# Optimization experiments

Measured on AMD Instinct MI355X. Metric: run time of the kernel, lower is better.

Reference implementation:

```python
import jax, jax.numpy as jnp
import numpy as np

N_NODES = 100000
N_EDGES = 1000000
IN_DIM = 64
HID = 64
N_CLUSTER = 30
REG = 0.01


def glorot(key, shape):
    lim = np.sqrt(6.0 / (shape[0] + shape[1]))
    return jax.random.uniform(key, shape, jnp.float32, -lim, lim)


def setup_inputs() -> dict:
    key = jax.random.key(0)
    k1, k2, k3, k4, k5 = jax.random.split(key, 5)
    x = jax.random.normal(k1, (N_NODES, IN_DIM), jnp.float32)
    edge_index = jax.random.randint(k2, (2, N_EDGES), 0, N_NODES, jnp.int64)
    edge_attr = jax.random.uniform(k3, (N_EDGES,), jnp.float32)
    W1 = glorot(k4, (IN_DIM, HID))
    b1 = jnp.zeros((HID,), jnp.float32)
    W2 = glorot(k5, (HID, N_CLUSTER))
    b2 = jnp.zeros((N_CLUSTER,), jnp.float32)
    return {"x": x, "edge_index": edge_index, "edge_attr": edge_attr,
            "W1": W1, "b1": b1, "W2": W2, "b2": b2}


def gcn_conv(x, W, b, src, dst, w):
    # PyG GCNConv with edge weights: add self-loops (weight 1), symmetric norm.
    h = x @ W  # [N, out]
    deg = jax.ops.segment_sum(w, dst, num_segments=N_NODES) + 1.0  # self-loop
    dinv = jax.lax.rsqrt(deg)
    norm = dinv[src] * w * dinv[dst]  # [E]
    agg = jax.ops.segment_sum(norm[:, None] * h[src], dst, num_segments=N_NODES)
    agg = agg + h / deg[:, None]  # self-loop contribution: norm = 1/deg
    return agg + b


def reference(x, edge_index, edge_attr, W1, b1, W2, b2):
    src, dst = edge_index[0], edge_index[1]
    h = jax.nn.relu(gcn_conv(x, W1, b1, src, dst, edge_attr))
    # dropout p=0 -> identity
    X2 = gcn_conv(h, W2, b2, src, dst, edge_attr)
    FX = jax.nn.softmax(X2, axis=-1)  # [N, C]
    FF = jnp.sum(FX[src] * FX[dst], axis=-1)  # [E]
    NFX = jnp.log(1.0 - FX ** 2)  # [N, C]
    preg = -jnp.sum(jnp.log(1.0001 - jnp.exp(jnp.sum(NFX, axis=0))))
    loss = jnp.mean((FF - edge_attr) ** 2)
    return FX, loss + REG * preg
```

## Files before the change

### kernel.cpp

```cpp
#include <hip/hip_runtime.h>
#include <hip/hip_fp16.h>
#include <math.h>

#define N_NODES 100000
#define N_EDGES 1000000
#define IN_DIM 64
#define HID 64
#define NC 30
#define NCP 32
#define REG_C 0.01f

#define NTILES (N_NODES / 16)
#define NBUCK 391
#define EPB_A 2048
#define NBLK_A 489
#define GEMM_BLOCKS 512

typedef _Float16 half8 __attribute__((ext_vector_type(8)));
typedef float f32x4 __attribute__((ext_vector_type(4)));

__device__ __forceinline__ unsigned char enc_fp8(float v) {
    return (unsigned char)(__builtin_amdgcn_cvt_pk_fp8_f32(v, v, 0, false) & 0xFF);
}
__device__ __forceinline__ float dec_fp8(unsigned char b) {
    return __builtin_amdgcn_cvt_f32_fp8((int)b, 0);
}
__device__ __forceinline__ float dot4_fp8(unsigned a, unsigned b) {
    float s = __builtin_amdgcn_cvt_f32_fp8((int)a, 0) * __builtin_amdgcn_cvt_f32_fp8((int)b, 0);
    s += __builtin_amdgcn_cvt_f32_fp8((int)a, 1) * __builtin_amdgcn_cvt_f32_fp8((int)b, 1);
    s += __builtin_amdgcn_cvt_f32_fp8((int)a, 2) * __builtin_amdgcn_cvt_f32_fp8((int)b, 2);
    s += __builtin_amdgcn_cvt_f32_fp8((int)a, 3) * __builtin_amdgcn_cvt_f32_fp8((int)b, 3);
    return s;
}

__global__ void hist_gemm(const int* __restrict__ dst, int* __restrict__ histT,
                          const float* __restrict__ X, const float* __restrict__ W,
                          unsigned char* __restrict__ H8) {
    if (blockIdx.x < NBLK_A) {
        __shared__ int cnt[NBUCK];
        for (int i = threadIdx.x; i < NBUCK; i += 256) cnt[i] = 0;
        __syncthreads();
        int e0 = blockIdx.x * EPB_A;
#pragma unroll
        for (int j = 0; j < 8; ++j) {
            int e = e0 + j * 256 + threadIdx.x;
            if (e < N_EDGES) atomicAdd(&cnt[dst[e] >> 8], 1);
        }
        __syncthreads();
        for (int b = threadIdx.x; b < NBUCK; b += 256)
            histT[b * NBLK_A + blockIdx.x] = cnt[b];
        return;
    }
    const int lane = threadIdx.x & 63;
    const int wave = threadIdx.x >> 6;
    const int qd = lane >> 4;
    const int l = lane & 15;
    half8 bfrag[2][4];
#pragma unroll
    for (int kb = 0; kb < 2; ++kb)
#pragma unroll
        for (int t = 0; t < 4; ++t)
#pragma unroll
            for (int j = 0; j < 8; ++j)
                bfrag[kb][t][j] = (_Float16)W[(kb * 32 + qd * 8 + j) * 64 + t * 16 + l];

    const int gb = blockIdx.x - NBLK_A;
    const int waveStride = GEMM_BLOCKS * 4;
    for (int ntile = gb * 4 + wave; ntile < NTILES; ntile += waveStride) {
        const int node0 = ntile * 16;
        const float* arow = X + (size_t)(node0 + l) * 64 + qd * 8;
        half8 af0, af1;
#pragma unroll
        for (int j = 0; j < 8; ++j) {
            af0[j] = (_Float16)arow[j];
            af1[j] = (_Float16)arow[32 + j];
        }
        f32x4 acc[4];
#pragma unroll
        for (int t = 0; t < 4; ++t) acc[t] = (f32x4){0.f, 0.f, 0.f, 0.f};
#pragma unroll
        for (int t = 0; t < 4; ++t) {
            acc[t] = __builtin_amdgcn_mfma_f32_16x16x32_f16(af0, bfrag[0][t], acc[t], 0, 0, 0);
            acc[t] = __builtin_amdgcn_mfma_f32_16x16x32_f16(af1, bfrag[1][t], acc[t], 0, 0, 0);
        }
#pragma unroll
        for (int t = 0; t < 4; ++t)
#pragma unroll
            for (int rr = 0; rr < 4; ++rr)
                H8[(size_t)(node0 + qd * 4 + rr) * 64 + t * 16 + l] = enc_fp8(acc[t][rr]);
    }
}

__global__ void scanA(int* __restrict__ histT, int* __restrict__ bucketTotal) {
    __shared__ int s[NBLK_A];
    int b = blockIdx.x;
    for (int i = threadIdx.x; i < NBLK_A; i += 256) s[i] = histT[b * NBLK_A + i];
    __syncthreads();
    if (threadIdx.x == 0) {
        int run = 0;
        for (int i = 0; i < NBLK_A; ++i) { int t = s[i]; s[i] = run; run += t; }
        bucketTotal[b] = run;
    }
    __syncthreads();
    for (int i = threadIdx.x; i < NBLK_A; i += 256) histT[b * NBLK_A + i] = s[i];
}

__global__ void scanB(const int* __restrict__ bucketTotal, int* __restrict__ bucketBase) {
    __shared__ int s[NBUCK];
    for (int i = threadIdx.x; i < NBUCK; i += 256) s[i] = bucketTotal[i];
    __syncthreads();
    if (threadIdx.x == 0) {
        int run = 0;
        for (int i = 0; i < NBUCK; ++i) { int t = s[i]; s[i] = run; run += t; }
    }
    __syncthreads();
    for (int i = threadIdx.x; i < NBUCK; i += 256) bucketBase[i] = s[i];
    if (threadIdx.x == 0) bucketBase[NBUCK] = N_EDGES;
}

__global__ void scatter_coarse(const int* __restrict__ src, const int* __restrict__ dst,
                               const float* __restrict__ w, const int* __restrict__ histT,
                               const int* __restrict__ bucketBase,
                               int2* __restrict__ sw, unsigned char* __restrict__ dl) {
    __shared__ int cur[NBUCK];
    int bl = blockIdx.x;
    for (int b = threadIdx.x; b < NBUCK; b += 256)
        cur[b] = bucketBase[b] + histT[b * NBLK_A + bl];
    __syncthreads();
    int e0 = bl * EPB_A;
#pragma unroll
    for (int j = 0; j < 8; ++j) {
        int e = e0 + j * 256 + threadIdx.x;
        if (e < N_EDGES) {
            int d = dst[e];
            int pos = atomicAdd(&cur[d >> 8], 1);
            sw[pos] = make_int2(src[e], __float_as_int(w[e]));
            dl[pos] = (unsigned char)(d & 255);
        }
    }
}

__global__ void bucket_deg(const int2* __restrict__ sw, const unsigned char* __restrict__ dl,
                           const int* __restrict__ bucketBase, float* __restrict__ dinv,
                           float* __restrict__ invdeg, int* __restrict__ rowptr) {
    __shared__ int cnt[256];
    __shared__ float degf[256];
    __shared__ int sc[256];
    int b = blockIdx.x, tid = threadIdx.x;
    cnt[tid] = 0; degf[tid] = 0.f;
    __syncthreads();
    int p0 = bucketBase[b], p1 = bucketBase[b + 1];
    for (int p = p0 + tid; p < p1; p += 256) {
        int d = dl[p];
        atomicAdd(&cnt[d], 1);
        atomicAdd(&degf[d], __int_as_float(sw[p].y));
    }
    __syncthreads();
    sc[tid] = cnt[tid];
    __syncthreads();
    for (int off = 1; off < 256; off <<= 1) {
        int t = (tid >= off) ? sc[tid - off] : 0;
        __syncthreads();
        sc[tid] += t;
        __syncthreads();
    }
    int node = b * 256 + tid;
    if (node < N_NODES) {
        float d = degf[tid] + 1.0f;
        dinv[node] = rsqrtf(d);
        invdeg[node] = 1.0f / d;
        rowptr[node] = p0 + sc[tid] - cnt[tid];
    }
    if (b == 0 && tid == 0) rowptr[N_NODES] = N_EDGES;
}

__global__ void bucket_scatter(const int2* __restrict__ sw, const unsigned char* __restrict__ dl,
                               const int* __restrict__ bucketBase, const int* __restrict__ rowptr,
                               const float* __restrict__ dinv,
                               int2* __restrict__ edata2, int2* __restrict__ wd) {
    __shared__ int cur[256];
    __shared__ float ldinv[256];
    int b = blockIdx.x, tid = threadIdx.x;
    int node = b * 256 + tid;
    if (node < N_NODES) { cur[tid] = rowptr[node]; ldinv[tid] = dinv[node]; }
    __syncthreads();
    int p0 = bucketBase[b], p1 = bucketBase[b + 1];
    for (int p = p0 + tid; p < p1; p += 256) {
        int d = dl[p];
        int2 r = sw[p];
        float wv = __int_as_float(r.y);
        float norm = dinv[r.x] * wv * ldinv[d];
        int pos = atomicAdd(&cur[d], 1);
        edata2[pos] = make_int2(r.x, __float_as_int(norm));
        wd[pos] = make_int2(r.y, b * 256 + d);
    }
}

__global__ void agg64_fused(const int* __restrict__ rowptr, const int2* __restrict__ edata2,
                            const unsigned char* __restrict__ H8, const float* __restrict__ invdeg,
                            const float* __restrict__ b1, _Float16* __restrict__ h2h) {
    int node = blockIdx.x * 4 + (threadIdx.x >> 6);
    int lane = threadIdx.x & 63;
    if (node >= N_NODES) return;
    int p = rowptr[node], end = rowptr[node + 1];
    float a0 = 0.f, a1 = 0.f, a2 = 0.f, a3 = 0.f;
    float a4 = 0.f, a5 = 0.f, a6 = 0.f, a7 = 0.f;
    for (; p + 7 < end; p += 8) {
        int2 e0 = edata2[p],     e1 = edata2[p + 1], e2 = edata2[p + 2], e3 = edata2[p + 3];
        int2 e4 = edata2[p + 4], e5 = edata2[p + 5], e6 = edata2[p + 6], e7 = edata2[p + 7];
        a0 += __int_as_float(e0.y) * dec_fp8(H8[(size_t)e0.x * 64 + lane]);
        a1 += __int_as_float(e1.y) * dec_fp8(H8[(size_t)e1.x * 64 + lane]);
        a2 += __int_as_float(e2.y) * dec_fp8(H8[(size_t)e2.x * 64 + lane]);
        a3 += __int_as_float(e3.y) * dec_fp8(H8[(size_t)e3.x * 64 + lane]);
        a4 += __int_as_float(e4.y) * dec_fp8(H8[(size_t)e4.x * 64 + lane]);
        a5 += __int_as_float(e5.y) * dec_fp8(H8[(size_t)e5.x * 64 + lane]);
        a6 += __int_as_float(e6.y) * dec_fp8(H8[(size_t)e6.x * 64 + lane]);
        a7 += __int_as_float(e7.y) * dec_fp8(H8[(size_t)e7.x * 64 + lane]);
    }
    for (; p + 1 < end; p += 2) {
        int2 e0 = edata2[p], e1 = edata2[p + 1];
        a0 += __int_as_float(e0.y) * dec_fp8(H8[(size_t)e0.x * 64 + lane]);
        a1 += __int_as_float(e1.y) * dec_fp8(H8[(size_t)e1.x * 64 + lane]);
    }
    if (p < end) {
        int2 e0 = edata2[p];
        a0 += __int_as_float(e0.y) * dec_fp8(H8[(size_t)e0.x * 64 + lane]);
    }
    float v = ((a0 + a1) + (a2 + a3)) + ((a4 + a5) + (a6 + a7)) +
              dec_fp8(H8[(size_t)node * 64 + lane]) * invdeg[node] + b1[lane];
    h2h[(size_t)node * 64 + lane] = (_Float16)fmaxf(v, 0.f);
}

__global__ void linear30(const _Float16* __restrict__ H, const float* __restrict__ W2,
                         __half* __restrict__ HH16) {
    __shared__ float sW[64 * NC];
    __shared__ float sH[8 * 64];
    for (int i = threadIdx.x; i < 64 * NC; i += blockDim.x) sW[i] = W2[i];
    int node0 = blockIdx.x * 8;
    for (int i = threadIdx.x; i < 8 * 64; i += blockDim.x) {
        int n = node0 + (i >> 6);
        sH[i] = (n < N_NODES) ? (float)H[(size_t)n * 64 + (i & 63)] : 0.f;
    }
    __syncthreads();
    int ln = threadIdx.x >> 5;
    int c = threadIdx.x & 31;
    int node = node0 + ln;
    if (node < N_NODES) {
        float acc = 0.f;
        if (c < NC) {
#pragma unroll
            for (int k = 0; k < 64; ++k) acc += sH[ln * 64 + k] * sW[k * NC + c];
        }
        HH16[(size_t)node * NCP + c] = __float2half(acc);
    }
}

__global__ void agg30_softmax_colsum(const int* __restrict__ rowptr, const int2* __restrict__ edata2,
                                     const __half* __restrict__ HH16,
                                     const float* __restrict__ invdeg,
                                     const float* __restrict__ b2, float* __restrict__ FX,
                                     unsigned char* __restrict__ FX8,
                                     float* __restrict__ colsum_part) {
    const int lane = threadIdx.x & 63;
    const int waveInBlock = threadIdx.x >> 6;
    const int half = lane >> 5;
    const int c = lane & 31;
    const bool activeC = (c < NC);
    const int wavesTotal = gridDim.x * (blockDim.x >> 6);
    const int w0 = blockIdx.x * (blockDim.x >> 6) + waveInBlock;

    const float bb = activeC ? b2[c] : 0.f;
    float lacc = 0.f;

    for (int pair = w0; pair < N_NODES / 2; pair += wavesTotal) {
        const int node = pair * 2 + half;
        int p = rowptr[node], end = rowptr[node + 1];
        float acc0 = 0.f, acc1 = 0.f, acc2 = 0.f, acc3 = 0.f;
        for (; p + 3 < end; p += 4) {
            int2 e0 = edata2[p],     e1 = edata2[p + 1];
            int2 e2 = edata2[p + 2], e3 = edata2[p + 3];
            acc0 += __int_as_float(e0.y) * __half2float(HH16[(size_t)e0.x * NCP + c]);
            acc1 += __int_as_float(e1.y) * __half2float(HH16[(size_t)e1.x * NCP + c]);
            acc2 += __int_as_float(e2.y) * __half2float(HH16[(size_t)e2.x * NCP + c]);
            acc3 += __int_as_float(e3.y) * __half2float(HH16[(size_t)e3.x * NCP + c]);
        }
        for (; p < end; ++p) {
            int2 e0 = edata2[p];
            acc0 += __int_as_float(e0.y) * __half2float(HH16[(size_t)e0.x * NCP + c]);
        }
        float selfv = __half2float(HH16[(size_t)node * NCP + c]);
        float x = activeC ? ((acc0 + acc1) + (acc2 + acc3) + selfv * invdeg[node] + bb)
                          : -INFINITY;
        float mx = x;
        for (int off = 16; off; off >>= 1) mx = fmaxf(mx, __shfl_xor(mx, off));
        float e = activeC ? expf(x - mx) : 0.f;
        float s = e;
        for (int off = 16; off; off >>= 1) s += __shfl_xor(s, off);
        float fx = e / s;
        if (activeC) {
            FX[(size_t)node * NC + c] = fx;
            FX8[(size_t)node * NCP + c] = enc_fp8(fx);
            lacc += log1pf(-fx * fx);
        } else {
            FX8[(size_t)node * NCP + c] = 0;
        }
    }
    lacc += __shfl_xor(lacc, 32);
    __shared__ float part[4][NC];
    if (half == 0 && activeC) part[waveInBlock][c] = lacc;
    __syncthreads();
    if (threadIdx.x < NC) {
        float v = part[0][threadIdx.x] + part[1][threadIdx.x] +
                  part[2][threadIdx.x] + part[3][threadIdx.x];
        atomicAdd(&colsum_part[(blockIdx.x & 63) * 32 + threadIdx.x], v);
    }
}

__global__ void edge_loss_sorted(const int2* __restrict__ edata2, const int2* __restrict__ wd,
                                 const unsigned char* __restrict__ FX8,
                                 float* __restrict__ mse_part) {
    int e = blockIdx.x * blockDim.x + threadIdx.x;
    float v = 0.f;
    if (e < N_EDGES) {
        int2 sn = edata2[e];
        int2 wdv = wd[e];
        const uint4* rs = (const uint4*)(FX8 + (size_t)sn.x * NCP);
        const uint4* rd = (const uint4*)(FX8 + (size_t)wdv.y * NCP);
        uint4 a0 = rs[0], a1 = rs[1];
        uint4 b0 = rd[0], b1 = rd[1];
        float ff = dot4_fp8(a0.x, b0.x) + dot4_fp8(a0.y, b0.y) +
                   dot4_fp8(a0.z, b0.z) + dot4_fp8(a0.w, b0.w) +
                   dot4_fp8(a1.x, b1.x) + dot4_fp8(a1.y, b1.y) +
                   dot4_fp8(a1.z, b1.z) + dot4_fp8(a1.w, b1.w);
        float diff = ff - __int_as_float(wdv.x);
        v = diff * diff;
    }
    for (int off = 32; off > 0; off >>= 1) v += __shfl_down(v, off);
    __shared__ float ps[4];
    int lane = threadIdx.x & 63, wv = threadIdx.x >> 6;
    if (lane == 0) ps[wv] = v;
    __syncthreads();
    if (threadIdx.x == 0)
        atomicAdd(&mse_part[blockIdx.x & 63], ps[0] + ps[1] + ps[2] + ps[3]);
}

__global__ void finalize(const float* __restrict__ colsum_part, const float* __restrict__ mse_part,
                         float* __restrict__ out_loss) {
    int t = threadIdx.x;
    float m = mse_part[t];
    for (int off = 32; off > 0; off >>= 1) m += __shfl_down(m, off);
    float term = 0.f;
    if (t < NC) {
        float s = 0.f;
        for (int k = 0; k < 64; ++k) s += colsum_part[k * 32 + t];
        term = logf(1.0001f - expf(s));
    }
    for (int off = 32; off > 0; off >>= 1) term += __shfl_down(term, off);
    if (t == 0)
        out_loss[0] = m / (float)N_EDGES - REG_C * term;
}

extern "C" void kernel_launch(void* const* d_in, const int* in_sizes, int n_in,
                              void* d_out, int out_size, void* d_ws, size_t ws_size,
                              hipStream_t stream) {
    const float* x  = (const float*)d_in[0];
    const int*   ei = (const int*)d_in[1];
    const float* ea = (const float*)d_in[2];
    const float* W1 = (const float*)d_in[3];
    const float* b1 = (const float*)d_in[4];
    const float* W2 = (const float*)d_in[5];
    const float* b2 = (const float*)d_in[6];
    const int* srcI = ei;
    const int* dstI = ei + N_EDGES;

    float* FX   = (float*)d_out;
    float* loss = FX + (size_t)N_NODES * NC;

    float* ws = (float*)d_ws;
    float*         dinv   = ws;
    float*         invdeg = ws + 100000;
    unsigned char* h8     = (unsigned char*)(ws + 200000);
    _Float16*      h2h    = (_Float16*)(ws + 1800000);
    __half*        hh16   = (__half*)(ws + 5000000);
    unsigned char* fx8    = (unsigned char*)(ws + 6600000);
    float*         colsum_part = ws + 7400000;
    float*         mse_part    = ws + 7402048;
    int*           rowptr = (int*)(ws + 7402112);
    int*           histT  = (int*)(ws + 7502114);
    int*           bucketTotal = (int*)(ws + 7693314);
    int*           bucketBase  = (int*)(ws + 7693706);
    int2*          sw     = (int2*)(ws + 7694098);
    unsigned char* dl     = (unsigned char*)(ws + 9694098);
    int2*          edata2 = (int2*)(ws + 9944098);
    int2*          wd     = (int2*)(ws + 11944098);

    hipMemsetAsync(colsum_part, 0, (2048 + 64) * sizeof(float), stream);

    hist_gemm<<<NBLK_A + GEMM_BLOCKS, 256, 0, stream>>>(dstI, histT, x, W1, h8);
    scanA<<<NBUCK, 256, 0, stream>>>(histT, bucketTotal);
    scanB<<<1, 256, 0, stream>>>(bucketTotal, bucketBase);
    scatter_coarse<<<NBLK_A, 256, 0, stream>>>(srcI, dstI, ea, histT, bucketBase, sw, dl);
    bucket_deg<<<NBUCK, 256, 0, stream>>>(sw, dl, bucketBase, dinv, invdeg, rowptr);
    bucket_scatter<<<NBUCK, 256, 0, stream>>>(sw, dl, bucketBase, rowptr, dinv, edata2, wd);
    agg64_fused<<<(N_NODES + 3) / 4, 256, 0, stream>>>(rowptr, edata2, h8, invdeg, b1, h2h);
    linear30<<<(N_NODES + 7) / 8, 256, 0, stream>>>(h2h, W2, hh16);
    agg30_softmax_colsum<<<4096, 256, 0, stream>>>(rowptr, edata2, hh16, invdeg, b2,
                                                   FX, fx8, colsum_part);
    edge_loss_sorted<<<(N_EDGES + 255) / 256, 256, 0, stream>>>(edata2, wd, fx8, mse_part);
    finalize<<<1, 64, 0, stream>>>(colsum_part, mse_part, loss);
}
```

Measured before the change: 303.9 us.

## Split wavefronts across edges with vector loads in both aggregation kernels

Both CSR aggregation kernels now split each wave into edge sub-groups. Each lane loads a 4-element packed slice of a neighbour row (4 fp8 bytes or 4 halves) instead of one scalar element, and partial sums are combined with cross-lane shuffles. This raises memory-level parallelism per wave and cuts the number of per-edge load instructions on the irregular gather. The softmax kernel now handles one node per wave, writes FX and packed FX8 from different lane groups, accumulates the column log-sums per lane with direct atomics instead of a shared-memory reduction, and is launched with half as many blocks. The cost is extra shuffle reductions and wasted lanes on short adjacency lists, since each wave processes edges in padded groups of 16.

```diff
diff --git a/kernel.cpp b/kernel.cpp
--- a/kernel.cpp
+++ b/kernel.cpp
@@ -17,13 +17,23 @@
 #define GEMM_BLOCKS 512
 
 typedef _Float16 half8 __attribute__((ext_vector_type(8)));
+typedef _Float16 h16x4 __attribute__((ext_vector_type(4)));
 typedef float f32x4 __attribute__((ext_vector_type(4)));
+typedef float f32x2 __attribute__((ext_vector_type(2)));
 
 __device__ __forceinline__ unsigned char enc_fp8(float v) {
     return (unsigned char)(__builtin_amdgcn_cvt_pk_fp8_f32(v, v, 0, false) & 0xFF);
 }
 __device__ __forceinline__ float dec_fp8(unsigned char b) {
     return __builtin_amdgcn_cvt_f32_fp8((int)b, 0);
+}
+__device__ __forceinline__ f32x4 dec_fp8x4(unsigned u) {
+    f32x4 r;
+    r[0] = __builtin_amdgcn_cvt_f32_fp8((int)u, 0);
+    r[1] = __builtin_amdgcn_cvt_f32_fp8((int)u, 1);
+    r[2] = __builtin_amdgcn_cvt_f32_fp8((int)u, 2);
+    r[3] = __builtin_amdgcn_cvt_f32_fp8((int)u, 3);
+    return r;
 }
 __device__ __forceinline__ float dot4_fp8(unsigned a, unsigned b) {
     float s = __builtin_amdgcn_cvt_f32_fp8((int)a, 0) * __builtin_amdgcn_cvt_f32_fp8((int)b, 0);
@@ -200,35 +210,71 @@
                             const unsigned char* __restrict__ H8, const float* __restrict__ invdeg,
                             const float* __restrict__ b1, _Float16* __restrict__ h2h) {
     int node = blockIdx.x * 4 + (threadIdx.x >> 6);
-    int lane = threadIdx.x & 63;
     if (node >= N_NODES) return;
+    const int lane = threadIdx.x & 63;
+    const int s = lane >> 4;
+    const int q = lane & 15;
     int p = rowptr[node], end = rowptr[node + 1];
-    float a0 = 0.f, a1 = 0.f, a2 = 0.f, a3 = 0.f;
-    float a4 = 0.f, a5 = 0.f, a6 = 0.f, a7 = 0.f;
-    for (; p + 7 < end; p += 8) {
-        int2 e0 = edata2[p],     e1 = edata2[p + 1], e2 = edata2[p + 2], e3 = edata2[p + 3];
-        int2 e4 = edata2[p + 4], e5 = edata2[p + 5], e6 = edata2[p + 6], e7 = edata2[p + 7];
-        a0 += __int_as_float(e0.y) * dec_fp8(H8[(size_t)e0.x * 64 + lane]);
-        a1 += __int_as_float(e1.y) * dec_fp8(H8[(size_t)e1.x * 64 + lane]);
-        a2 += __int_as_float(e2.y) * dec_fp8(H8[(size_t)e2.x * 64 + lane]);
-        a3 += __int_as_float(e3.y) * dec_fp8(H8[(size_t)e3.x * 64 + lane]);
-        a4 += __int_as_float(e4.y) * dec_fp8(H8[(size_t)e4.x * 64 + lane]);
-        a5 += __int_as_float(e5.y) * dec_fp8(H8[(size_t)e5.x * 64 + lane]);
-        a6 += __int_as_float(e6.y) * dec_fp8(H8[(size_t)e6.x * 64 + lane]);
-        a7 += __int_as_float(e7.y) * dec_fp8(H8[(size_t)e7.x * 64 + lane]);
-    }
-    for (; p + 1 < end; p += 2) {
-        int2 e0 = edata2[p], e1 = edata2[p + 1];
-        a0 += __int_as_float(e0.y) * dec_fp8(H8[(size_t)e0.x * 64 + lane]);
-        a1 += __int_as_float(e1.y) * dec_fp8(H8[(size_t)e1.x * 64 + lane]);
-    }
-    if (p < end) {
-        int2 e0 = edata2[p];
-        a0 += __int_as_float(e0.y) * dec_fp8(H8[(size_t)e0.x * 64 + lane]);
-    }
-    float v = ((a0 + a1) + (a2 + a3)) + ((a4 + a5) + (a6 + a7)) +
-              dec_fp8(H8[(size_t)node * 64 + lane]) * invdeg[node] + b1[lane];
-    h2h[(size_t)node * 64 + lane] = (_Float16)fmaxf(v, 0.f);
+    float acc[4][4] = {};
+    for (; p + 15 < end; p += 16) {
+        int2 e[4];
+#pragma unroll
+        for (int g = 0; g < 4; ++g) e[g] = edata2[p + 4 * g + s];
+        unsigned u[4];
+#pragma unroll
+        for (int g = 0; g < 4; ++g)
+            u[g] = *(const unsigned*)(H8 + ((unsigned)e[g].x << 6) + (q << 2));
+#pragma unroll
+        for (int g = 0; g < 4; ++g) {
+            float n = __int_as_float(e[g].y);
+            f32x4 d = dec_fp8x4(u[g]);
+#pragma unroll
+            for (int j = 0; j < 4; ++j)
+                acc[g][j] += n * d[j];
+        }
+    }
+    {
+        int r = end - p;
+        int2 e[4];
+#pragma unroll
+        for (int g = 0; g < 4; ++g) {
+            e[g] = make_int2(0, 0);
+            if (4 * g + s < r) e[g] = edata2[p + 4 * g + s];
+        }
+        unsigned u[4];
+#pragma unroll
+        for (int g = 0; g < 4; ++g)
+            u[g] = *(const unsigned*)(H8 + ((unsigned)e[g].x << 6) + (q << 2));
+#pragma unroll
+        for (int g = 0; g < 4; ++g) {
+            float n = __int_as_float(e[g].y);
+            f32x4 d = dec_fp8x4(u[g]);
+#pragma unroll
+            for (int j = 0; j < 4; ++j)
+                acc[g][j] += n * d[j];
+        }
+    }
+    float v[4];
+#pragma unroll
+    for (int j = 0; j < 4; ++j) {
+        float t = (acc[0][j] + acc[1][j]) + (acc[2][j] + acc[3][j]);
+        t += __shfl_xor(t, 16);
+        t += __shfl_xor(t, 32);
+        v[j] = t;
+    }
+    unsigned us = *(const unsigned*)(H8 + ((unsigned)node << 6) + (q << 2));
+    float idg = invdeg[node];
+    f32x4 bv = *(const f32x4*)(b1 + (q << 2));
+    if (s == 0) {
+        f32x4 ds = dec_fp8x4(us);
+        h16x4 hv;
+#pragma unroll
+        for (int j = 0; j < 4; ++j) {
+            float rj = v[j] + ds[j] * idg + bv[j];
+            hv[j] = (_Float16)fmaxf(rj, 0.f);
+        }
+        *(h16x4*)(h2h + ((unsigned)node << 6) + (q << 2)) = hv;
+    }
 }
 
 __global__ void linear30(const _Float16* __restrict__ H, const float* __restrict__ W2,
@@ -262,57 +308,95 @@
                                      unsigned char* __restrict__ FX8,
                                      float* __restrict__ colsum_part) {
     const int lane = threadIdx.x & 63;
-    const int waveInBlock = threadIdx.x >> 6;
-    const int half = lane >> 5;
-    const int c = lane & 31;
-    const bool activeC = (c < NC);
+    const int s = lane >> 3;
+    const int q = lane & 7;
     const int wavesTotal = gridDim.x * (blockDim.x >> 6);
-    const int w0 = blockIdx.x * (blockDim.x >> 6) + waveInBlock;
-
-    const float bb = activeC ? b2[c] : 0.f;
-    float lacc = 0.f;
-
-    for (int pair = w0; pair < N_NODES / 2; pair += wavesTotal) {
-        const int node = pair * 2 + half;
+    const int w0 = blockIdx.x * (blockDim.x >> 6) + (threadIdx.x >> 6);
+
+    float bb[4];
+#pragma unroll
+    for (int j = 0; j < 4; ++j) bb[j] = (4 * q + j < NC) ? b2[4 * q + j] : 0.f;
+    float lacc[4] = {0.f, 0.f, 0.f, 0.f};
+
+    for (int node = w0; node < N_NODES; node += wavesTotal) {
         int p = rowptr[node], end = rowptr[node + 1];
-        float acc0 = 0.f, acc1 = 0.f, acc2 = 0.f, acc3 = 0.f;
-        for (; p + 3 < end; p += 4) {
-            int2 e0 = edata2[p],     e1 = edata2[p + 1];
-            int2 e2 = edata2[p + 2], e3 = edata2[p + 3];
-            acc0 += __int_as_float(e0.y) * __half2float(HH16[(size_t)e0.x * NCP + c]);
-            acc1 += __int_as_float(e1.y) * __half2float(HH16[(size_t)e1.x * NCP + c]);
-            acc2 += __int_as_float(e2.y) * __half2float(HH16[(size_t)e2.x * NCP + c]);
-            acc3 += __int_as_float(e3.y) * __half2float(HH16[(size_t)e3.x * NCP + c]);
-        }
-        for (; p < end; ++p) {
-            int2 e0 = edata2[p];
-            acc0 += __int_as_float(e0.y) * __half2float(HH16[(size_t)e0.x * NCP + c]);
-        }
-        float selfv = __half2float(HH16[(size_t)node * NCP + c]);
-        float x = activeC ? ((acc0 + acc1) + (acc2 + acc3) + selfv * invdeg[node] + bb)
-                          : -INFINITY;
-        float mx = x;
-        for (int off = 16; off; off >>= 1) mx = fmaxf(mx, __shfl_xor(mx, off));
-        float e = activeC ? expf(x - mx) : 0.f;
-        float s = e;
-        for (int off = 16; off; off >>= 1) s += __shfl_xor(s, off);
-        float fx = e / s;
-        if (activeC) {
-            FX[(size_t)node * NC + c] = fx;
-            FX8[(size_t)node * NCP + c] = enc_fp8(fx);
-            lacc += log1pf(-fx * fx);
-        } else {
-            FX8[(size_t)node * NCP + c] = 0;
-        }
-    }
-    lacc += __shfl_xor(lacc, 32);
-    __shared__ float part[4][NC];
-    if (half == 0 && activeC) part[waveInBlock][c] = lacc;
-    __syncthreads();
-    if (threadIdx.x < NC) {
-        float v = part[0][threadIdx.x] + part[1][threadIdx.x] +
-                  part[2][threadIdx.x] + part[3][threadIdx.x];
-        atomicAdd(&colsum_part[(blockIdx.x & 63) * 32 + threadIdx.x], v);
+        float a0[4] = {}, a1[4] = {};
+        for (; p + 15 < end; p += 16) {
+            int2 e0 = edata2[p + s];
+            int2 e1 = edata2[p + 8 + s];
+            h16x4 h0 = *(const h16x4*)(HH16 + ((unsigned)e0.x << 5) + (q << 2));
+            h16x4 h1 = *(const h16x4*)(HH16 + ((unsigned)e1.x << 5) + (q << 2));
+            float n0 = __int_as_float(e0.y), n1 = __int_as_float(e1.y);
+#pragma unroll
+            for (int j = 0; j < 4; ++j) {
+                a0[j] += n0 * (float)h0[j];
+                a1[j] += n1 * (float)h1[j];
+            }
+        }
+        {
+            int r = end - p;
+            int2 e0 = make_int2(0, 0), e1 = make_int2(0, 0);
+            if (s < r) e0 = edata2[p + s];
+            if (s + 8 < r) e1 = edata2[p + 8 + s];
+            h16x4 h0 = *(const h16x4*)(HH16 + ((unsigned)e0.x << 5) + (q << 2));
+            h16x4 h1 = *(const h16x4*)(HH16 + ((unsigned)e1.x << 5) + (q << 2));
+            float n0 = __int_as_float(e0.y), n1 = __int_as_float(e1.y);
+#pragma unroll
+            for (int j = 0; j < 4; ++j) {
+                a0[j] += n0 * (float)h0[j];
+                a1[j] += n1 * (float)h1[j];
+            }
+        }
+        h16x4 hs = *(const h16x4*)(HH16 + ((unsigned)node << 5) + (q << 2));
+        float idg = invdeg[node];
+        float x[4];
+#pragma unroll
+        for (int j = 0; j < 4; ++j) {
+            float t = a0[j] + a1[j];
+            t += __shfl_xor(t, 8);
+            t += __shfl_xor(t, 16);
+            t += __shfl_xor(t, 32);
+            x[j] = (4 * q + j < NC) ? (t + (float)hs[j] * idg + bb[j]) : -INFINITY;
+        }
+        float mx = fmaxf(fmaxf(x[0], x[1]), fmaxf(x[2], x[3]));
+        mx = fmaxf(mx, __shfl_xor(mx, 1));
+        mx = fmaxf(mx, __shfl_xor(mx, 2));
+        mx = fmaxf(mx, __shfl_xor(mx, 4));
+        float e[4];
+        float sum = 0.f;
+#pragma unroll
+        for (int j = 0; j < 4; ++j) {
+            e[j] = (4 * q + j < NC) ? expf(x[j] - mx) : 0.f;
+            sum += e[j];
+        }
+        sum += __shfl_xor(sum, 1);
+        sum += __shfl_xor(sum, 2);
+        sum += __shfl_xor(sum, 4);
+        float invs = 1.0f / sum;
+        float fx[4];
+#pragma unroll
+        for (int j = 0; j < 4; ++j) fx[j] = e[j] * invs;
+
+        if (s == 0) {
+            *(f32x2*)(FX + (size_t)node * NC + 4 * q) = (f32x2){fx[0], fx[1]};
+        } else if (s == 1) {
+            if (q < 7)
+                *(f32x2*)(FX + (size_t)node * NC + 4 * q + 2) = (f32x2){fx[2], fx[3]};
+        } else if (s == 2) {
+            unsigned pk = (unsigned)enc_fp8(fx[0]) | ((unsigned)enc_fp8(fx[1]) << 8);
+            if (4 * q + 2 < NC) pk |= ((unsigned)enc_fp8(fx[2]) << 16);
+            if (4 * q + 3 < NC) pk |= ((unsigned)enc_fp8(fx[3]) << 24);
+            *(unsigned*)(FX8 + ((unsigned)node << 5) + (q << 2)) = pk;
+        }
+#pragma unroll
+        for (int j = 0; j < 4; ++j)
+            if (4 * q + j < NC) { float f = fx[j]; lacc[j] += log1pf(-f * f); }
+    }
+    if (s == 0) {
+#pragma unroll
+        for (int j = 0; j < 4; ++j)
+            if (4 * q + j < NC)
+                atomicAdd(&colsum_part[(blockIdx.x & 63) * 32 + 4 * q + j], lacc[j]);
     }
 }
 
@@ -404,7 +488,7 @@
     bucket_scatter<<<NBUCK, 256, 0, stream>>>(sw, dl, bucketBase, rowptr, dinv, edata2, wd);
     agg64_fused<<<(N_NODES + 3) / 4, 256, 0, stream>>>(rowptr, edata2, h8, invdeg, b1, h2h);
     linear30<<<(N_NODES + 7) / 8, 256, 0, stream>>>(h2h, W2, hh16);
-    agg30_softmax_colsum<<<4096, 256, 0, stream>>>(rowptr, edata2, hh16, invdeg, b2,
+    agg30_softmax_colsum<<<2048, 256, 0, stream>>>(rowptr, edata2, hh16, invdeg, b2,
                                                    FX, fx8, colsum_part);
     edge_loss_sorted<<<(N_EDGES + 255) / 256, 256, 0, stream>>>(edata2, wd, fx8, mse_part);
     finalize<<<1, 64, 0, stream>>>(colsum_part, mse_part, loss);
```

Result: slower. 361.4 us (+18.9%).
